# Performance work log

Hardware: AMD Instinct MI355X
Metric: run time of the kernel (lower is better)

## Reference

```python
import jax, jax.numpy as jnp
import numpy as np

B, T, C, H = 4, 2048, 1024, 16
D = C // H
SCALE = float(np.sqrt(C / H))  # quadf_scale = sqrt(D) = 8.0


def setup_inputs() -> dict:
    key = jax.random.key(0)
    k1, k2, k3 = jax.random.split(key, 3)
    x = jax.random.normal(k1, (B, T, C), dtype=jnp.float32)
    # torch Linear(C, 3C): y = x @ W.T; we store the transposed weight [C, 3C]
    W_attn = jax.random.normal(k2, (C, 3 * C), dtype=jnp.float32) * 0.02
    W_proj = jax.random.normal(k3, (C, C), dtype=jnp.float32) * 0.02
    return {"x": x, "W_attn": W_attn, "W_proj": W_proj}


def reference(x, W_attn, W_proj):
    # QKV projection
    qkv = x @ W_attn                      # [B, T, 3C]
    q, k, v = jnp.split(qkv, 3, axis=-1)  # each [B, T, C]

    def heads(t):  # [B, T, C] -> [B, H, T, D]
        return t.reshape(B, T, H, D).transpose(0, 2, 1, 3)

    q, k, v = heads(q), heads(k), heads(v)

    # scaled dot-product scores with causal mask
    scores = jnp.einsum("bhtd,bhsd->bhts", q, k) / SCALE  # [B, H, T, T]
    causal = jnp.tril(jnp.ones((T, T), dtype=bool))
    scores = jnp.where(causal, scores, -jnp.inf)
    attn = jax.nn.softmax(scores, axis=-1)
    # dropout = 0.0 (eval mode), so omitted

    y = jnp.einsum("bhts,bhsd->bhtd", attn, v)            # [B, H, T, D]
    y = y.transpose(0, 2, 1, 3).reshape(B, T, C)
    return y @ W_proj
```

## Files before the change

kernel.cpp:

```cpp
#include <hip/hip_runtime.h>
#include <hip/hip_bf16.h>

#define B_ 4
#define T_ 2048
#define C_ 1024
#define H_ 16
#define D_ 64
#define C3 3072

typedef __bf16 bf16x8 __attribute__((ext_vector_type(8)));
typedef __bf16 bf16x4 __attribute__((ext_vector_type(4)));
typedef float f32x2 __attribute__((ext_vector_type(2)));
typedef float f32x4 __attribute__((ext_vector_type(4)));
typedef float f32x16 __attribute__((ext_vector_type(16)));
typedef unsigned u32x4 __attribute__((ext_vector_type(4)));

#define SCALE_LOG2E 0.1803368801111244f

__device__ __forceinline__ void gload_lds16(const void* g, void* lds) {
  __builtin_amdgcn_global_load_lds((const __attribute__((address_space(1))) void*)g,
                                   (__attribute__((address_space(3))) void*)lds, 16, 0, 0);
}

__device__ __forceinline__ int swz128(int row, int chunk) {
  return row * 128 + ((chunk ^ (row & 7)) << 4);
}

__device__ __forceinline__ unsigned cvt_pk_bf16(float a, float b) {
  unsigned r;
  asm("v_cvt_pk_bf16_f32 %0, %1, %2" : "=v"(r) : "v"(a), "v"(b));
  return r;
}

__device__ __forceinline__ void pl32swap(unsigned& x, unsigned& y) {
  asm volatile("v_permlane32_swap_b32 %0, %1" : "+v"(x), "+v"(y));
}

__device__ __forceinline__ float fmax3(float a, float b, float c) {
  float d;
  asm("v_max3_f32 %0, %1, %2, %3" : "=v"(d) : "v"(a), "v"(b), "v"(c));
  return d;
}

__device__ __forceinline__ f32x2 pk_add(f32x2 a, f32x2 b) {
  f32x2 d;
  asm("v_pk_add_f32 %0, %1, %2" : "=v"(d) : "v"(a), "v"(b));
  return d;
}

__global__ __launch_bounds__(256) void prep_kernel(const float* __restrict__ x,
                                                   const float* __restrict__ Wa,
                                                   const float* __restrict__ Wp,
                                                   __bf16* __restrict__ xb,
                                                   __bf16* __restrict__ wat,
                                                   __bf16* __restrict__ wpt) {
  __shared__ float tile[32][33];
  int bid = blockIdx.x, tid = threadIdx.x;
  if (bid < 8192) {
    int i = bid * 256 + tid;
    float4 v = ((const float4*)x)[i];
    bf16x4 o;
    o.x = (__bf16)v.x; o.y = (__bf16)v.y; o.z = (__bf16)v.z; o.w = (__bf16)v.w;
    ((bf16x4*)xb)[i] = o;
    return;
  }
  const float* in;
  __bf16* out;
  int N, bx, by;
  if (bid < 11264) {
    int lb = bid - 8192;
    in = Wa; out = wat; N = C3;
    bx = lb % 96; by = lb / 96;
  } else {
    int lb = bid - 11264;
    in = Wp; out = wpt; N = C_;
    bx = lb & 31; by = lb >> 5;
  }
  int K = C_;
  int kb = by * 32, nb = bx * 32;
  int tx = tid & 31, ty = tid >> 5;
#pragma unroll
  for (int i = 0; i < 4; i++) {
    int r = ty + i * 8;
    tile[r][tx] = in[(size_t)(kb + r) * N + nb + tx];
  }
  __syncthreads();
#pragma unroll
  for (int i = 0; i < 4; i++) {
    int r = ty + i * 8;
    out[(size_t)(nb + r) * K + kb + tx] = (__bf16)tile[tx][r];
  }
}

template <int MODE>
__global__ __launch_bounds__(256) void gemm_bt_kernel(const __bf16* __restrict__ A,
                                                      const __bf16* __restrict__ Bt,
                                                      __bf16* __restrict__ Cb,
                                                      float* __restrict__ Cf,
                                                      __bf16* __restrict__ vT,
                                                      int M, int N, int K) {
  __shared__ __align__(16) char lds[2][32768];
  int tid = threadIdx.x, w = tid >> 6, l = tid & 63;
  int gx = gridDim.x;
  int nwg = gx * gridDim.y;
  int orig = blockIdx.y * gx + blockIdx.x;
  int cpx = nwg >> 3;
  int swz = (orig & 7) * cpx + (orig >> 3);
  int bx = swz % gx, by = swz / gx;
  int m0 = by * 128, n0 = bx * 128;
  int wr = w >> 1, wc = w & 1;
  int lr = l & 15, lhi = l >> 4;

  int srow = l >> 3;
  int cg = (l & 7) ^ (srow & 7);

  f32x4 acc[4][4];
#pragma unroll
  for (int m = 0; m < 4; m++)
#pragma unroll
    for (int n = 0; n < 4; n++) acc[m][n] = (f32x4){0.f, 0.f, 0.f, 0.f};

  auto stage = [&](int kt, int buf) {
    int k0 = kt << 6;
    char* la = &lds[buf][0];
    char* lb = &lds[buf][16384];
#pragma unroll
    for (int jj = 0; jj < 4; jj++) {
      int q = w * 4 + jj;
      int row = q * 8 + srow;
      gload_lds16(A + (size_t)(m0 + row) * K + k0 + cg * 8, la + q * 1024);
      gload_lds16(Bt + (size_t)(n0 + row) * K + k0 + cg * 8, lb + q * 1024);
    }
  };

  int nK = K >> 6;
  stage(0, 0);

  for (int kt = 0; kt < nK; kt++) {
    int buf = kt & 1;
    __syncthreads();
    if (kt + 1 < nK) stage(kt + 1, buf ^ 1);
    char* la = &lds[buf][0];
    char* lb = &lds[buf][16384];

    bf16x8 af[4][2], bfr[4][2];
#pragma unroll
    for (int m = 0; m < 4; m++) {
      int r = wr * 64 + m * 16 + lr;
#pragma unroll
      for (int kc = 0; kc < 2; kc++)
        af[m][kc] = *(const bf16x8*)(la + swz128(r, kc * 4 + lhi));
    }
#pragma unroll
    for (int n = 0; n < 4; n++) {
      int r = wc * 64 + n * 16 + lr;
#pragma unroll
      for (int kc = 0; kc < 2; kc++)
        bfr[n][kc] = *(const bf16x8*)(lb + swz128(r, kc * 4 + lhi));
    }
#pragma unroll
    for (int kc = 0; kc < 2; kc++)
#pragma unroll
      for (int m = 0; m < 4; m++)
#pragma unroll
        for (int n = 0; n < 4; n++)
          acc[m][n] =
              __builtin_amdgcn_mfma_f32_16x16x32_bf16(af[m][kc], bfr[n][kc], acc[m][n], 0, 0, 0);
  }

  if (MODE == 2 && n0 >= 2048) {
    int bb = m0 >> 11;
    int tb = (m0 & 2047) + wr * 64 + lhi * 4;
#pragma unroll
    for (int n = 0; n < 4; n++) {
      int vcol = (n0 - 2048) + wc * 64 + n * 16 + lr;
      __bf16* vp = vT + ((size_t)bb * 1024 + vcol) * T_;
#pragma unroll
      for (int m = 0; m < 4; m++) {
        bf16x4 pv;
#pragma unroll
        for (int i = 0; i < 4; i++) pv[i] = (__bf16)acc[m][n][i];
        *(bf16x4*)(vp + tb + m * 16) = pv;
      }
    }
    return;
  }

  float oscale = (MODE == 2 && n0 < 1024) ? SCALE_LOG2E : 1.0f;
#pragma unroll
  for (int m = 0; m < 4; m++)
#pragma unroll
    for (int n = 0; n < 4; n++)
#pragma unroll
      for (int i = 0; i < 4; i++) {
        int rg = m0 + wr * 64 + m * 16 + lhi * 4 + i;
        int cg2 = n0 + wc * 64 + n * 16 + lr;
        if (MODE == 1)
          Cf[(size_t)rg * N + cg2] = acc[m][n][i];
        else
          Cb[(size_t)rg * N + cg2] = (__bf16)(acc[m][n][i] * oscale);
      }
}

__global__ __launch_bounds__(256) void attn_kernel(const __bf16* __restrict__ qkv,
                                                   const __bf16* __restrict__ vT,
                                                   __bf16* __restrict__ y) {
  __shared__ __align__(16) char lds[2][16384];
  int tid = threadIdx.x, w = tid >> 6, l = tid & 63;

  int g = blockIdx.x >> 6, bh = blockIdx.x & 63;
  int q2 = g >> 2;
  int qb = (q2 & 1) ? ((q2 == 1) ? g + 4 : g - 12) : (15 - g);
  int b = bh >> 4, h = bh & 15;
  size_t base = (size_t)b * T_ * C3;
  int lq = l & 31, hi = l >> 5;
  int qrow = qb * 128 + w * 32 + lq;
  int q0w = qb * 128 + w * 32;

  int lrow = l >> 3;
  int cg = (l & 7) ^ (lrow & 7);
  const __bf16* kptr = qkv + base + (size_t)(w * 16 + lrow) * C3 + C_ + h * D_ + cg * 8;
  const __bf16* vptr = vT + ((size_t)bh * D_ + w * 16 + lrow) * T_ + cg * 8;

  bf16x8 qf[4];
  {
    const __bf16* qp = qkv + base + (size_t)qrow * C3 + h * D_;
#pragma unroll
    for (int c = 0; c < 4; c++) qf[c] = *(const bf16x8*)(qp + c * 16 + hi * 8);
  }

  f32x16 zacc;
#pragma unroll
  for (int i = 0; i < 16; i++) zacc[i] = 0.f;
  f32x16 o[2];
  o[0] = zacc; o[1] = zacc;
  float mrun = -__builtin_inff(), lrun = 0.f;

  int nt = 2 * qb + 2;

  {
    char* kb = &lds[0][0];
    char* vb = &lds[0][8192];
    gload_lds16(kptr, kb + w * 2048);
    gload_lds16(kptr + 8 * C3, kb + w * 2048 + 1024);
    gload_lds16(vptr, vb + w * 2048);
    gload_lds16(vptr + 8 * T_, vb + w * 2048 + 1024);
  }

  for (int kt = 0; kt < nt; kt++) {
    int buf = kt & 1;
    __syncthreads();
    if (kt + 1 < nt) {
      char* kb = &lds[buf ^ 1][0];
      char* vb = &lds[buf ^ 1][8192];
      const __bf16* kp = kptr + (size_t)(kt + 1) * 64 * C3;
      const __bf16* vp = vptr + (kt + 1) * 64;
      gload_lds16(kp, kb + w * 2048);
      gload_lds16(kp + 8 * C3, kb + w * 2048 + 1024);
      gload_lds16(vp, vb + w * 2048);
      gload_lds16(vp + 8 * T_, vb + w * 2048 + 1024);
    }
    if (kt * 64 > q0w + 31) continue;
    char* kb = &lds[buf][0];
    char* vb = &lds[buf][8192];

    f32x16 s[2];
    __builtin_amdgcn_s_setprio(1);
#pragma unroll
    for (int b2 = 0; b2 < 2; b2++) {
      bf16x8 kf0 = *(const bf16x8*)(kb + swz128(b2 * 32 + lq, hi));
      s[b2] = __builtin_amdgcn_mfma_f32_32x32x16_bf16(kf0, qf[0], zacc, 0, 0, 0);
#pragma unroll
      for (int c = 1; c < 4; c++) {
        bf16x8 kf = *(const bf16x8*)(kb + swz128(b2 * 32 + lq, 2 * c + hi));
        s[b2] = __builtin_amdgcn_mfma_f32_32x32x16_bf16(kf, qf[c], s[b2], 0, 0, 0);
      }
    }
    __builtin_amdgcn_s_setprio(0);

    if (kt * 64 + 63 > q0w) {
#pragma unroll
      for (int b2 = 0; b2 < 2; b2++)
#pragma unroll
        for (int r = 0; r < 16; r++) {
          int kv = kt * 64 + b2 * 32 + ((r & 3) + 8 * (r >> 2)) + 4 * hi;
          if (kv > qrow) s[b2][r] = -1e30f;
        }
    }

    {
      auto xi = [&](int i) -> float { return i < 16 ? s[0][i] : s[1][i - 16]; };
      float t10[11];
#pragma unroll
      for (int g3 = 0; g3 < 10; g3++) t10[g3] = fmax3(xi(3 * g3), xi(3 * g3 + 1), xi(3 * g3 + 2));
      t10[10] = fmaxf(xi(30), xi(31));
      float u0 = fmax3(t10[0], t10[1], t10[2]);
      float u1 = fmax3(t10[3], t10[4], t10[5]);
      float u2 = fmax3(t10[6], t10[7], t10[8]);
      float u3 = fmaxf(t10[9], t10[10]);
      float tl = fmaxf(fmax3(u0, u1, u2), u3);
      float tmax = fmaxf(tl, __shfl_xor(tl, 32));

      if (!__all(tmax - mrun <= 8.0f)) {
        float mnew = fmaxf(mrun, tmax);
        float al = __builtin_amdgcn_exp2f(mrun - mnew);
        mrun = mnew;
        lrun *= al;
#pragma unroll
        for (int d = 0; d < 2; d++)
#pragma unroll
          for (int i = 0; i < 16; i++) o[d][i] *= al;
      }
    }

#pragma unroll
    for (int b2 = 0; b2 < 2; b2++)
#pragma unroll
      for (int r = 0; r < 16; r++) s[b2][r] = __builtin_amdgcn_exp2f(s[b2][r] - mrun);

    {
      f32x2 p8[8];
#pragma unroll
      for (int g3 = 0; g3 < 8; g3++) {
        f32x2 a = {s[0][2 * g3], s[0][2 * g3 + 1]};
        f32x2 b2v = {s[1][2 * g3], s[1][2 * g3 + 1]};
        p8[g3] = pk_add(a, b2v);
      }
#pragma unroll
      for (int g3 = 0; g3 < 4; g3++) p8[g3] = pk_add(p8[g3], p8[g3 + 4]);
      p8[0] = pk_add(p8[0], p8[2]);
      p8[1] = pk_add(p8[1], p8[3]);
      p8[0] = pk_add(p8[0], p8[1]);
      float rs = p8[0][0] + p8[0][1];
      lrun += rs + __shfl_xor(rs, 32);
    }

    bf16x8 pa[4];
#pragma unroll
    for (int b2 = 0; b2 < 2; b2++) {
      unsigned wg[4][2];
#pragma unroll
      for (int gg = 0; gg < 4; gg++) {
        wg[gg][0] = cvt_pk_bf16(s[b2][4 * gg + 0], s[b2][4 * gg + 1]);
        wg[gg][1] = cvt_pk_bf16(s[b2][4 * gg + 2], s[b2][4 * gg + 3]);
      }
#pragma unroll
      for (int cp = 0; cp < 2; cp++) {
        unsigned x0 = wg[2 * cp][0], x1 = wg[2 * cp][1];
        unsigned y0 = wg[2 * cp + 1][0], y1 = wg[2 * cp + 1][1];
        pl32swap(x0, y0);
        pl32swap(x1, y1);
        union { u32x4 u; bf16x8 hh; } uu;
        uu.u = (u32x4){x0, x1, y0, y1};
        pa[b2 * 2 + cp] = uu.hh;
      }
    }

    __builtin_amdgcn_s_setprio(1);
#pragma unroll
    for (int db = 0; db < 2; db++)
#pragma unroll
      for (int c = 0; c < 4; c++) {
        bf16x8 vf = *(const bf16x8*)(vb + swz128(db * 32 + lq, 2 * c + hi));
        o[db] = __builtin_amdgcn_mfma_f32_32x32x16_bf16(vf, pa[c], o[db], 0, 0, 0);
      }
    __builtin_amdgcn_s_setprio(0);
  }

  float inv = 1.f / lrun;
  __bf16* yp = y + (size_t)(b * T_ + qrow) * C_ + h * D_;
#pragma unroll
  for (int db = 0; db < 2; db++)
#pragma unroll
    for (int rr = 0; rr < 4; rr++) {
      bf16x4 ov;
#pragma unroll
      for (int i = 0; i < 4; i++) ov[i] = (__bf16)(o[db][rr * 4 + i] * inv);
      *(bf16x4*)(yp + db * 32 + rr * 8 + hi * 4) = ov;
    }
}

extern "C" void kernel_launch(void* const* d_in, const int* in_sizes, int n_in,
                              void* d_out, int out_size, void* d_ws, size_t ws_size,
                              hipStream_t stream) {
  const float* x = (const float*)d_in[0];
  const float* Wa = (const float*)d_in[1];
  const float* Wp = (const float*)d_in[2];
  float* out = (float*)d_out;
  char* ws = (char*)d_ws;

  __bf16* xb  = (__bf16*)(ws);
  __bf16* yb  = (__bf16*)(ws);
  __bf16* wat = (__bf16*)(ws + 16777216);
  __bf16* wpt = (__bf16*)(ws + 23068672);
  __bf16* qkv = (__bf16*)(ws + 25165824);
  __bf16* vT  = (__bf16*)(ws + 75497472);

  prep_kernel<<<12288, 256, 0, stream>>>(x, Wa, Wp, xb, wat, wpt);

  gemm_bt_kernel<2><<<dim3(C3 / 128, (B_ * T_) / 128), 256, 0, stream>>>(
      xb, wat, qkv, nullptr, vT, B_ * T_, C3, C_);

  attn_kernel<<<dim3(1024), 256, 0, stream>>>(qkv, vT, yb);

  gemm_bt_kernel<1><<<dim3(C_ / 128, (B_ * T_) / 128), 256, 0, stream>>>(
      yb, wpt, nullptr, out, nullptr, B_ * T_, C_, C_);
}
```

Before: 151.7 us.

## Restructure attention into paired causal query tiles with smaller two-wave blocks

The attention kernel now uses 128-thread blocks that each process two 64-row query tiles (j and 31-j), so every block does the same amount of causal work. This replaces the 128-row tiles over four waves and the remapped block order. The double-buffered K/V prefetch is dropped: each tile is loaded into a single LDS buffer with a synchronous load, bracketed by two barriers. Blocks are also interleaved across XCDs by a bid remap. The intent is better load balance and occupancy, at the cost of exposing global load latency with no overlap and loading each K/V tile for only 64 query rows.

```diff
diff --git a/kernel.cpp b/kernel.cpp
--- a/kernel.cpp
+++ b/kernel.cpp
@@ -202,182 +202,170 @@
       }
 }
 
-__global__ __launch_bounds__(256) void attn_kernel(const __bf16* __restrict__ qkv,
+__global__ __launch_bounds__(128) void attn_kernel(const __bf16* __restrict__ qkv,
                                                    const __bf16* __restrict__ vT,
                                                    __bf16* __restrict__ y) {
-  __shared__ __align__(16) char lds[2][16384];
+  __shared__ __align__(16) char lds[16384];
   int tid = threadIdx.x, w = tid >> 6, l = tid & 63;
-
-  int g = blockIdx.x >> 6, bh = blockIdx.x & 63;
-  int q2 = g >> 2;
-  int qb = (q2 & 1) ? ((q2 == 1) ? g + 4 : g - 12) : (15 - g);
-  int b = bh >> 4, h = bh & 15;
+  int bid = blockIdx.x;
+  int lin = (bid & 7) * 128 + (bid >> 3);
+  int j = lin & 15, bh = lin >> 4, b = bh >> 4, h = bh & 15;
   size_t base = (size_t)b * T_ * C3;
   int lq = l & 31, hi = l >> 5;
-  int qrow = qb * 128 + w * 32 + lq;
-  int q0w = qb * 128 + w * 32;
 
   int lrow = l >> 3;
   int cg = (l & 7) ^ (lrow & 7);
-  const __bf16* kptr = qkv + base + (size_t)(w * 16 + lrow) * C3 + C_ + h * D_ + cg * 8;
-  const __bf16* vptr = vT + ((size_t)bh * D_ + w * 16 + lrow) * T_ + cg * 8;
-
-  bf16x8 qf[4];
-  {
-    const __bf16* qp = qkv + base + (size_t)qrow * C3 + h * D_;
-#pragma unroll
-    for (int c = 0; c < 4; c++) qf[c] = *(const bf16x8*)(qp + c * 16 + hi * 8);
-  }
+  const __bf16* kbase = qkv + base + (size_t)(w * 32 + lrow) * C3 + C_ + h * D_ + cg * 8;
+  const __bf16* vbase = vT + ((size_t)bh * D_ + w * 32 + lrow) * T_ + cg * 8;
+  char* kb = lds;
+  char* vb = lds + 8192;
 
   f32x16 zacc;
 #pragma unroll
   for (int i = 0; i < 16; i++) zacc[i] = 0.f;
-  f32x16 o[2];
-  o[0] = zacc; o[1] = zacc;
-  float mrun = -__builtin_inff(), lrun = 0.f;
-
-  int nt = 2 * qb + 2;
-
-  {
-    char* kb = &lds[0][0];
-    char* vb = &lds[0][8192];
-    gload_lds16(kptr, kb + w * 2048);
-    gload_lds16(kptr + 8 * C3, kb + w * 2048 + 1024);
-    gload_lds16(vptr, vb + w * 2048);
-    gload_lds16(vptr + 8 * T_, vb + w * 2048 + 1024);
-  }
-
-  for (int kt = 0; kt < nt; kt++) {
-    int buf = kt & 1;
-    __syncthreads();
-    if (kt + 1 < nt) {
-      char* kb = &lds[buf ^ 1][0];
-      char* vb = &lds[buf ^ 1][8192];
-      const __bf16* kp = kptr + (size_t)(kt + 1) * 64 * C3;
-      const __bf16* vp = vptr + (kt + 1) * 64;
-      gload_lds16(kp, kb + w * 2048);
-      gload_lds16(kp + 8 * C3, kb + w * 2048 + 1024);
-      gload_lds16(vp, vb + w * 2048);
-      gload_lds16(vp + 8 * T_, vb + w * 2048 + 1024);
-    }
-    if (kt * 64 > q0w + 31) continue;
-    char* kb = &lds[buf][0];
-    char* vb = &lds[buf][8192];
-
-    f32x16 s[2];
-    __builtin_amdgcn_s_setprio(1);
-#pragma unroll
-    for (int b2 = 0; b2 < 2; b2++) {
-      bf16x8 kf0 = *(const bf16x8*)(kb + swz128(b2 * 32 + lq, hi));
-      s[b2] = __builtin_amdgcn_mfma_f32_32x32x16_bf16(kf0, qf[0], zacc, 0, 0, 0);
-#pragma unroll
-      for (int c = 1; c < 4; c++) {
-        bf16x8 kf = *(const bf16x8*)(kb + swz128(b2 * 32 + lq, 2 * c + hi));
-        s[b2] = __builtin_amdgcn_mfma_f32_32x32x16_bf16(kf, qf[c], s[b2], 0, 0, 0);
-      }
-    }
-    __builtin_amdgcn_s_setprio(0);
-
-    if (kt * 64 + 63 > q0w) {
+
+#pragma unroll 1
+  for (int pi = 0; pi < 2; pi++) {
+    int p = pi ? (31 - j) : j;
+    int qrow = p * 64 + w * 32 + lq;
+
+    bf16x8 qf[4];
+    {
+      const __bf16* qp = qkv + base + (size_t)qrow * C3 + h * D_;
+#pragma unroll
+      for (int c = 0; c < 4; c++) qf[c] = *(const bf16x8*)(qp + c * 16 + hi * 8);
+    }
+
+    f32x16 o[2];
+    o[0] = zacc; o[1] = zacc;
+    float mrun = -__builtin_inff(), lrun = 0.f;
+
+#pragma unroll 1
+    for (int kt = 0; kt <= p; kt++) {
+      __syncthreads();
+#pragma unroll
+      for (int jj = 0; jj < 4; jj++) {
+        gload_lds16(kbase + (size_t)(kt * 64 + jj * 8) * C3, kb + w * 4096 + jj * 1024);
+        gload_lds16(vbase + (size_t)(jj * 8) * T_ + kt * 64, vb + w * 4096 + jj * 1024);
+      }
+      __syncthreads();
+
+      f32x16 s[2];
+      __builtin_amdgcn_s_setprio(1);
+#pragma unroll
+      for (int b2 = 0; b2 < 2; b2++) {
+        bf16x8 kf0 = *(const bf16x8*)(kb + swz128(b2 * 32 + lq, hi));
+        s[b2] = __builtin_amdgcn_mfma_f32_32x32x16_bf16(kf0, qf[0], zacc, 0, 0, 0);
+#pragma unroll
+        for (int c = 1; c < 4; c++) {
+          bf16x8 kf = *(const bf16x8*)(kb + swz128(b2 * 32 + lq, 2 * c + hi));
+          s[b2] = __builtin_amdgcn_mfma_f32_32x32x16_bf16(kf, qf[c], s[b2], 0, 0, 0);
+        }
+      }
+      __builtin_amdgcn_s_setprio(0);
+
+      if (kt == p) {
+#pragma unroll
+        for (int b2 = 0; b2 < 2; b2++)
+#pragma unroll
+          for (int r = 0; r < 16; r++) {
+            int kv = kt * 64 + b2 * 32 + ((r & 3) + 8 * (r >> 2)) + 4 * hi;
+            if (kv > qrow) s[b2][r] = -1e30f;
+          }
+      }
+
+      {
+        auto xi = [&](int i) -> float { return i < 16 ? s[0][i] : s[1][i - 16]; };
+        float t10[11];
+#pragma unroll
+        for (int g3 = 0; g3 < 10; g3++)
+          t10[g3] = fmax3(xi(3 * g3), xi(3 * g3 + 1), xi(3 * g3 + 2));
+        t10[10] = fmaxf(xi(30), xi(31));
+        float u0 = fmax3(t10[0], t10[1], t10[2]);
+        float u1 = fmax3(t10[3], t10[4], t10[5]);
+        float u2 = fmax3(t10[6], t10[7], t10[8]);
+        float u3 = fmaxf(t10[9], t10[10]);
+        float tl = fmaxf(fmax3(u0, u1, u2), u3);
+        float tmax = fmaxf(tl, __shfl_xor(tl, 32));
+
+        if (!__all(tmax - mrun <= 8.0f)) {
+          float mnew = fmaxf(mrun, tmax);
+          float al = __builtin_amdgcn_exp2f(mrun - mnew);
+          mrun = mnew;
+          lrun *= al;
+#pragma unroll
+          for (int d = 0; d < 2; d++)
+#pragma unroll
+            for (int i = 0; i < 16; i++) o[d][i] *= al;
+        }
+      }
+
 #pragma unroll
       for (int b2 = 0; b2 < 2; b2++)
 #pragma unroll
-        for (int r = 0; r < 16; r++) {
-          int kv = kt * 64 + b2 * 32 + ((r & 3) + 8 * (r >> 2)) + 4 * hi;
-          if (kv > qrow) s[b2][r] = -1e30f;
-        }
-    }
-
-    {
-      auto xi = [&](int i) -> float { return i < 16 ? s[0][i] : s[1][i - 16]; };
-      float t10[11];
-#pragma unroll
-      for (int g3 = 0; g3 < 10; g3++) t10[g3] = fmax3(xi(3 * g3), xi(3 * g3 + 1), xi(3 * g3 + 2));
-      t10[10] = fmaxf(xi(30), xi(31));
-      float u0 = fmax3(t10[0], t10[1], t10[2]);
-      float u1 = fmax3(t10[3], t10[4], t10[5]);
-      float u2 = fmax3(t10[6], t10[7], t10[8]);
-      float u3 = fmaxf(t10[9], t10[10]);
-      float tl = fmaxf(fmax3(u0, u1, u2), u3);
-      float tmax = fmaxf(tl, __shfl_xor(tl, 32));
-
-      if (!__all(tmax - mrun <= 8.0f)) {
-        float mnew = fmaxf(mrun, tmax);
-        float al = __builtin_amdgcn_exp2f(mrun - mnew);
-        mrun = mnew;
-        lrun *= al;
-#pragma unroll
-        for (int d = 0; d < 2; d++)
-#pragma unroll
-          for (int i = 0; i < 16; i++) o[d][i] *= al;
-      }
-    }
-
-#pragma unroll
-    for (int b2 = 0; b2 < 2; b2++)
-#pragma unroll
-      for (int r = 0; r < 16; r++) s[b2][r] = __builtin_amdgcn_exp2f(s[b2][r] - mrun);
-
-    {
-      f32x2 p8[8];
-#pragma unroll
-      for (int g3 = 0; g3 < 8; g3++) {
-        f32x2 a = {s[0][2 * g3], s[0][2 * g3 + 1]};
-        f32x2 b2v = {s[1][2 * g3], s[1][2 * g3 + 1]};
-        p8[g3] = pk_add(a, b2v);
-      }
-#pragma unroll
-      for (int g3 = 0; g3 < 4; g3++) p8[g3] = pk_add(p8[g3], p8[g3 + 4]);
-      p8[0] = pk_add(p8[0], p8[2]);
-      p8[1] = pk_add(p8[1], p8[3]);
-      p8[0] = pk_add(p8[0], p8[1]);
-      float rs = p8[0][0] + p8[0][1];
-      lrun += rs + __shfl_xor(rs, 32);
-    }
-
-    bf16x8 pa[4];
-#pragma unroll
-    for (int b2 = 0; b2 < 2; b2++) {
-      unsigned wg[4][2];
-#pragma unroll
-      for (int gg = 0; gg < 4; gg++) {
-        wg[gg][0] = cvt_pk_bf16(s[b2][4 * gg + 0], s[b2][4 * gg + 1]);
-        wg[gg][1] = cvt_pk_bf16(s[b2][4 * gg + 2], s[b2][4 * gg + 3]);
-      }
-#pragma unroll
-      for (int cp = 0; cp < 2; cp++) {
-        unsigned x0 = wg[2 * cp][0], x1 = wg[2 * cp][1];
-        unsigned y0 = wg[2 * cp + 1][0], y1 = wg[2 * cp + 1][1];
-        pl32swap(x0, y0);
-        pl32swap(x1, y1);
-        union { u32x4 u; bf16x8 hh; } uu;
-        uu.u = (u32x4){x0, x1, y0, y1};
-        pa[b2 * 2 + cp] = uu.hh;
-      }
-    }
-
-    __builtin_amdgcn_s_setprio(1);
+        for (int r = 0; r < 16; r++) s[b2][r] = __builtin_amdgcn_exp2f(s[b2][r] - mrun);
+
+      {
+        f32x2 p8[8];
+#pragma unroll
+        for (int g3 = 0; g3 < 8; g3++) {
+          f32x2 a = {s[0][2 * g3], s[0][2 * g3 + 1]};
+          f32x2 b2v = {s[1][2 * g3], s[1][2 * g3 + 1]};
+          p8[g3] = pk_add(a, b2v);
+        }
+#pragma unroll
+        for (int g3 = 0; g3 < 4; g3++) p8[g3] = pk_add(p8[g3], p8[g3 + 4]);
+        p8[0] = pk_add(p8[0], p8[2]);
+        p8[1] = pk_add(p8[1], p8[3]);
+        p8[0] = pk_add(p8[0], p8[1]);
+        float rs = p8[0][0] + p8[0][1];
+        lrun += rs + __shfl_xor(rs, 32);
+      }
+
+      bf16x8 pa[4];
+#pragma unroll
+      for (int b2 = 0; b2 < 2; b2++) {
+        unsigned wg[4][2];
+#pragma unroll
+        for (int gg = 0; gg < 4; gg++) {
+          wg[gg][0] = cvt_pk_bf16(s[b2][4 * gg + 0], s[b2][4 * gg + 1]);
+          wg[gg][1] = cvt_pk_bf16(s[b2][4 * gg + 2], s[b2][4 * gg + 3]);
+        }
+#pragma unroll
+        for (int cp = 0; cp < 2; cp++) {
+          unsigned x0 = wg[2 * cp][0], x1 = wg[2 * cp][1];
+          unsigned y0 = wg[2 * cp + 1][0], y1 = wg[2 * cp + 1][1];
+          pl32swap(x0, y0);
+          pl32swap(x1, y1);
+          union { u32x4 u; bf16x8 hh; } uu;
+          uu.u = (u32x4){x0, x1, y0, y1};
+          pa[b2 * 2 + cp] = uu.hh;
+        }
+      }
+
+      __builtin_amdgcn_s_setprio(1);
+#pragma unroll
+      for (int db = 0; db < 2; db++)
+#pragma unroll
+        for (int c = 0; c < 4; c++) {
+          bf16x8 vf = *(const bf16x8*)(vb + swz128(db * 32 + lq, 2 * c + hi));
+          o[db] = __builtin_amdgcn_mfma_f32_32x32x16_bf16(vf, pa[c], o[db], 0, 0, 0);
+        }
+      __builtin_amdgcn_s_setprio(0);
+    }
+
+    float inv = 1.f / lrun;
+    __bf16* yp = y + (size_t)(b * T_ + qrow) * C_ + h * D_;
 #pragma unroll
     for (int db = 0; db < 2; db++)
 #pragma unroll
-      for (int c = 0; c < 4; c++) {
-        bf16x8 vf = *(const bf16x8*)(vb + swz128(db * 32 + lq, 2 * c + hi));
-        o[db] = __builtin_amdgcn_mfma_f32_32x32x16_bf16(vf, pa[c], o[db], 0, 0, 0);
-      }
-    __builtin_amdgcn_s_setprio(0);
-  }
-
-  float inv = 1.f / lrun;
-  __bf16* yp = y + (size_t)(b * T_ + qrow) * C_ + h * D_;
-#pragma unroll
-  for (int db = 0; db < 2; db++)
-#pragma unroll
-    for (int rr = 0; rr < 4; rr++) {
-      bf16x4 ov;
-#pragma unroll
-      for (int i = 0; i < 4; i++) ov[i] = (__bf16)(o[db][rr * 4 + i] * inv);
-      *(bf16x4*)(yp + db * 32 + rr * 8 + hi * 4) = ov;
-    }
+      for (int rr = 0; rr < 4; rr++) {
+        bf16x4 ov;
+#pragma unroll
+        for (int i = 0; i < 4; i++) ov[i] = (__bf16)(o[db][rr * 4 + i] * inv);
+        *(bf16x4*)(yp + db * 32 + rr * 8 + hi * 4) = ov;
+      }
+  }
 }
 
 extern "C" void kernel_launch(void* const* d_in, const int* in_sizes, int n_in,
@@ -401,7 +389,7 @@
   gemm_bt_kernel<2><<<dim3(C3 / 128, (B_ * T_) / 128), 256, 0, stream>>>(
       xb, wat, qkv, nullptr, vT, B_ * T_, C3, C_);
 
-  attn_kernel<<<dim3(1024), 256, 0, stream>>>(qkv, vT, yb);
+  attn_kernel<<<dim3(1024), 128, 0, stream>>>(qkv, vT, yb);
 
   gemm_bt_kernel<1><<<dim3(C_ / 128, (B_ * T_) / 128), 256, 0, stream>>>(
       yb, wpt, nullptr, out, nullptr, B_ * T_, C_, C_);
```

New measurement: 164.8 us. 8.6% more time.

## Add 256x256-tile 8-wave QKV GEMM with phased async LDS pipeline

Applied to the files above, without the earlier changes.

Replaces the 128x128 QKV projection GEMM with a dedicated 512-thread kernel using 256x256 output tiles, 128KB LDS double buffering, and fine-grained per-quadrant staging with explicit vmcnt waits and setprio around MFMA blocks. Larger tiles raise arithmetic intensity and cut global/L2 traffic per FLOP, and the interleaved schedule overlaps loads with MFMA. The grid shrinks to 12x32=384 workgroups with one block per CU due to LDS use, which risks lower occupancy and tail imbalance. The output projection GEMM is simplified to fp32-only.

```diff
diff --git a/kernel.cpp b/kernel.cpp
--- a/kernel.cpp
+++ b/kernel.cpp
@@ -92,12 +92,147 @@
   }
 }
 
-template <int MODE>
+__global__ __launch_bounds__(512) void gemm_qkv256_kernel(const __bf16* __restrict__ A,
+                                                          const __bf16* __restrict__ Bt,
+                                                          __bf16* __restrict__ Cb,
+                                                          __bf16* __restrict__ vT,
+                                                          int M, int N, int K) {
+  __shared__ __align__(16) char lds[131072];
+  int tid = threadIdx.x, w = tid >> 6, l = tid & 63;
+  int wm = w >> 2, wn = w & 3;
+  int lr = l & 15, lhi = l >> 4;
+
+  int gx = gridDim.x;
+  int nwg = gx * gridDim.y;
+  int orig = blockIdx.y * gx + blockIdx.x;
+  int cpx = nwg >> 3;
+  int swz = (orig & 7) * cpx + (orig >> 3);
+  int bx = swz % gx, by = swz / gx;
+  int m0 = by * 256, n0 = bx * 256;
+
+  const __bf16* Abase = A + (size_t)m0 * K;
+  const __bf16* Bbase = Bt + (size_t)n0 * K;
+
+  f32x4 acc[8][4];
+#pragma unroll
+  for (int m = 0; m < 8; m++)
+#pragma unroll
+    for (int n = 0; n < 4; n++) acc[m][n] = (f32x4){0.f, 0.f, 0.f, 0.f};
+
+  int nKtot = K >> 6;
+  int lrow = l >> 3;
+  int cgs = (l & 7) ^ lrow;
+
+  auto stageu = [&](int u, int kt, int bufb) {
+    if (kt >= nKtot) kt = nKtot - 1;
+    int k0 = kt << 6;
+    char* dA = lds + bufb * 65536;
+    char* dB = dA + 32768;
+#pragma unroll
+    for (int jj = 0; jj < 2; jj++) {
+      int j = w * 2 + jj;
+      if (u == 0 || u == 3) {
+        int q = (u == 3);
+        int rowbase = (j >> 3) * 128 + q * 64 + (j & 7) * 8;
+        gload_lds16(Abase + (size_t)(rowbase + lrow) * K + k0 + cgs * 8, dA + rowbase * 128);
+      } else {
+        int q = (u == 2);
+        int rowbase = (j >> 2) * 64 + q * 32 + (j & 3) * 8;
+        gload_lds16(Bbase + (size_t)(rowbase + lrow) * K + k0 + cgs * 8, dB + rowbase * 128);
+      }
+    }
+  };
+
+  stageu(0, 0, 0);
+  stageu(1, 0, 0);
+  stageu(2, 0, 0);
+  stageu(3, 0, 0);
+  asm volatile("s_waitcnt vmcnt(4)" ::: "memory");
+  __builtin_amdgcn_s_barrier();
+
+  int nIter = nKtot >> 1;
+  for (int it = 0; it < nIter; it++) {
+    int tS1 = 2 * it + 1;
+    int tS2 = 2 * it + 2;
+#pragma unroll
+    for (int ph = 0; ph < 8; ph++) {
+      const int grp = ph >> 2;
+      const int sub = ph & 3;
+      const int QM = sub >> 1, QN = sub & 1;
+      if (sub == 0)      asm volatile("s_waitcnt vmcnt(4)" ::: "memory");
+      else if (sub == 1) asm volatile("s_waitcnt vmcnt(6)" ::: "memory");
+      else if (sub == 2) asm volatile("s_waitcnt vmcnt(6)" ::: "memory");
+      char* lA = lds + grp * 65536;
+      char* lB = lA + 32768;
+      bf16x8 af[4][2], bfr[2][2];
+#pragma unroll
+      for (int mf = 0; mf < 4; mf++)
+#pragma unroll
+        for (int kk = 0; kk < 2; kk++)
+          af[mf][kk] =
+              *(const bf16x8*)(lA + swz128(wm * 128 + QM * 64 + mf * 16 + lr, kk * 4 + lhi));
+#pragma unroll
+      for (int nf = 0; nf < 2; nf++)
+#pragma unroll
+        for (int kk = 0; kk < 2; kk++)
+          bfr[nf][kk] =
+              *(const bf16x8*)(lB + swz128(wn * 64 + QN * 32 + nf * 16 + lr, kk * 4 + lhi));
+      {
+        int tS = grp == 0 ? tS1 : tS2;
+        int dstb = grp == 0 ? 1 : 0;
+        if (sub == 0) { stageu(0, tS, dstb); stageu(1, tS, dstb); }
+        else if (sub == 1) stageu(2, tS, dstb);
+        else if (sub == 2) stageu(3, tS, dstb);
+      }
+      __builtin_amdgcn_s_barrier();
+      __builtin_amdgcn_s_setprio(1);
+#pragma unroll
+      for (int kk = 0; kk < 2; kk++)
+#pragma unroll
+        for (int mf = 0; mf < 4; mf++)
+#pragma unroll
+          for (int nf = 0; nf < 2; nf++)
+            acc[QM * 4 + mf][QN * 2 + nf] = __builtin_amdgcn_mfma_f32_16x16x32_bf16(
+                af[mf][kk], bfr[nf][kk], acc[QM * 4 + mf][QN * 2 + nf], 0, 0, 0);
+      __builtin_amdgcn_s_setprio(0);
+      __builtin_amdgcn_s_barrier();
+    }
+  }
+
+  if (n0 >= 2048) {
+    int bb = m0 >> 11;
+    int tb = (m0 & 2047) + wm * 128 + lhi * 4;
+#pragma unroll
+    for (int n = 0; n < 4; n++) {
+      int vcol = (n0 - 2048) + wn * 64 + n * 16 + lr;
+      __bf16* vp = vT + ((size_t)bb * 1024 + vcol) * T_;
+#pragma unroll
+      for (int m = 0; m < 8; m++) {
+        bf16x4 pv;
+#pragma unroll
+        for (int i = 0; i < 4; i++) pv[i] = (__bf16)acc[m][n][i];
+        *(bf16x4*)(vp + tb + m * 16) = pv;
+      }
+    }
+    return;
+  }
+
+  float oscale = (n0 < 1024) ? SCALE_LOG2E : 1.0f;
+#pragma unroll
+  for (int m = 0; m < 8; m++)
+#pragma unroll
+    for (int n = 0; n < 4; n++)
+#pragma unroll
+      for (int i = 0; i < 4; i++) {
+        int rg = m0 + wm * 128 + m * 16 + lhi * 4 + i;
+        int cg2 = n0 + wn * 64 + n * 16 + lr;
+        Cb[(size_t)rg * N + cg2] = (__bf16)(acc[m][n][i] * oscale);
+      }
+}
+
 __global__ __launch_bounds__(256) void gemm_bt_kernel(const __bf16* __restrict__ A,
                                                       const __bf16* __restrict__ Bt,
-                                                      __bf16* __restrict__ Cb,
                                                       float* __restrict__ Cf,
-                                                      __bf16* __restrict__ vT,
                                                       int M, int N, int K) {
   __shared__ __align__(16) char lds[2][32768];
   int tid = threadIdx.x, w = tid >> 6, l = tid & 63;
@@ -168,25 +303,6 @@
               __builtin_amdgcn_mfma_f32_16x16x32_bf16(af[m][kc], bfr[n][kc], acc[m][n], 0, 0, 0);
   }
 
-  if (MODE == 2 && n0 >= 2048) {
-    int bb = m0 >> 11;
-    int tb = (m0 & 2047) + wr * 64 + lhi * 4;
-#pragma unroll
-    for (int n = 0; n < 4; n++) {
-      int vcol = (n0 - 2048) + wc * 64 + n * 16 + lr;
-      __bf16* vp = vT + ((size_t)bb * 1024 + vcol) * T_;
-#pragma unroll
-      for (int m = 0; m < 4; m++) {
-        bf16x4 pv;
-#pragma unroll
-        for (int i = 0; i < 4; i++) pv[i] = (__bf16)acc[m][n][i];
-        *(bf16x4*)(vp + tb + m * 16) = pv;
-      }
-    }
-    return;
-  }
-
-  float oscale = (MODE == 2 && n0 < 1024) ? SCALE_LOG2E : 1.0f;
 #pragma unroll
   for (int m = 0; m < 4; m++)
 #pragma unroll
@@ -195,10 +311,7 @@
       for (int i = 0; i < 4; i++) {
         int rg = m0 + wr * 64 + m * 16 + lhi * 4 + i;
         int cg2 = n0 + wc * 64 + n * 16 + lr;
-        if (MODE == 1)
-          Cf[(size_t)rg * N + cg2] = acc[m][n][i];
-        else
-          Cb[(size_t)rg * N + cg2] = (__bf16)(acc[m][n][i] * oscale);
+        Cf[(size_t)rg * N + cg2] = acc[m][n][i];
       }
 }
 
@@ -398,11 +511,11 @@
 
   prep_kernel<<<12288, 256, 0, stream>>>(x, Wa, Wp, xb, wat, wpt);
 
-  gemm_bt_kernel<2><<<dim3(C3 / 128, (B_ * T_) / 128), 256, 0, stream>>>(
-      xb, wat, qkv, nullptr, vT, B_ * T_, C3, C_);
+  gemm_qkv256_kernel<<<dim3(C3 / 256, (B_ * T_) / 256), 512, 0, stream>>>(
+      xb, wat, qkv, vT, B_ * T_, C3, C_);
 
   attn_kernel<<<dim3(1024), 256, 0, stream>>>(qkv, vT, yb);
 
-  gemm_bt_kernel<1><<<dim3(C_ / 128, (B_ * T_) / 128), 256, 0, stream>>>(
-      yb, wpt, nullptr, out, nullptr, B_ * T_, C_, C_);
-}
+  gemm_bt_kernel<<<dim3(C_ / 128, (B_ * T_) / 128), 256, 0, stream>>>(
+      yb, wpt, out, B_ * T_, C_, C_);
+}
```

New measurement: 165.6 us. +9.2%, slower.

## Split attention into 64-row query blocks with two-wave workgroups

Applied to the files above, without the earlier changes.

Reorganizes the causal attention kernel from 1024 workgroups of 4 waves (128 query rows) to 2048 workgroups of 2 waves (64 query rows). Each wave now loads twice as much K/V per tile, and the per-wave skip of fully masked tiles is dropped because tile counts match the query block exactly. Blocks are ordered longest-first with a simpler scheduling map. The aim is finer-grained load balance and less wasted work on masked tiles, at the cost of K/V tiles being reloaded by twice as many workgroups.

```diff
diff --git a/kernel.cpp b/kernel.cpp
--- a/kernel.cpp
+++ b/kernel.cpp
@@ -202,25 +202,23 @@
       }
 }
 
-__global__ __launch_bounds__(256) void attn_kernel(const __bf16* __restrict__ qkv,
+__global__ __launch_bounds__(128) void attn_kernel(const __bf16* __restrict__ qkv,
                                                    const __bf16* __restrict__ vT,
                                                    __bf16* __restrict__ y) {
   __shared__ __align__(16) char lds[2][16384];
   int tid = threadIdx.x, w = tid >> 6, l = tid & 63;
-
-  int g = blockIdx.x >> 6, bh = blockIdx.x & 63;
-  int q2 = g >> 2;
-  int qb = (q2 & 1) ? ((q2 == 1) ? g + 4 : g - 12) : (15 - g);
+  int p = 31 - (blockIdx.x >> 6);
+  int bh = blockIdx.x & 63;
   int b = bh >> 4, h = bh & 15;
   size_t base = (size_t)b * T_ * C3;
   int lq = l & 31, hi = l >> 5;
-  int qrow = qb * 128 + w * 32 + lq;
-  int q0w = qb * 128 + w * 32;
+  int qrow = p * 64 + w * 32 + lq;
+  int q0w = p * 64 + w * 32;
 
   int lrow = l >> 3;
   int cg = (l & 7) ^ (lrow & 7);
-  const __bf16* kptr = qkv + base + (size_t)(w * 16 + lrow) * C3 + C_ + h * D_ + cg * 8;
-  const __bf16* vptr = vT + ((size_t)bh * D_ + w * 16 + lrow) * T_ + cg * 8;
+  const __bf16* kptr = qkv + base + (size_t)(w * 32 + lrow) * C3 + C_ + h * D_ + cg * 8;
+  const __bf16* vptr = vT + ((size_t)bh * D_ + w * 32 + lrow) * T_ + cg * 8;
 
   bf16x8 qf[4];
   {
@@ -236,17 +234,19 @@
   o[0] = zacc; o[1] = zacc;
   float mrun = -__builtin_inff(), lrun = 0.f;
 
-  int nt = 2 * qb + 2;
+  int nt = p + 1;
 
   {
     char* kb = &lds[0][0];
     char* vb = &lds[0][8192];
-    gload_lds16(kptr, kb + w * 2048);
-    gload_lds16(kptr + 8 * C3, kb + w * 2048 + 1024);
-    gload_lds16(vptr, vb + w * 2048);
-    gload_lds16(vptr + 8 * T_, vb + w * 2048 + 1024);
-  }
-
+#pragma unroll
+    for (int jj = 0; jj < 4; jj++) {
+      gload_lds16(kptr + (size_t)(jj * 8) * C3, kb + w * 4096 + jj * 1024);
+      gload_lds16(vptr + (size_t)(jj * 8) * T_, vb + w * 4096 + jj * 1024);
+    }
+  }
+
+#pragma unroll 1
   for (int kt = 0; kt < nt; kt++) {
     int buf = kt & 1;
     __syncthreads();
@@ -255,12 +255,12 @@
       char* vb = &lds[buf ^ 1][8192];
       const __bf16* kp = kptr + (size_t)(kt + 1) * 64 * C3;
       const __bf16* vp = vptr + (kt + 1) * 64;
-      gload_lds16(kp, kb + w * 2048);
-      gload_lds16(kp + 8 * C3, kb + w * 2048 + 1024);
-      gload_lds16(vp, vb + w * 2048);
-      gload_lds16(vp + 8 * T_, vb + w * 2048 + 1024);
-    }
-    if (kt * 64 > q0w + 31) continue;
+#pragma unroll
+      for (int jj = 0; jj < 4; jj++) {
+        gload_lds16(kp + (size_t)(jj * 8) * C3, kb + w * 4096 + jj * 1024);
+        gload_lds16(vp + (size_t)(jj * 8) * T_, vb + w * 4096 + jj * 1024);
+      }
+    }
     char* kb = &lds[buf][0];
     char* vb = &lds[buf][8192];
 
@@ -401,7 +401,7 @@
   gemm_bt_kernel<2><<<dim3(C3 / 128, (B_ * T_) / 128), 256, 0, stream>>>(
       xb, wat, qkv, nullptr, vT, B_ * T_, C3, C_);
 
-  attn_kernel<<<dim3(1024), 256, 0, stream>>>(qkv, vT, yb);
+  attn_kernel<<<dim3(2048), 128, 0, stream>>>(qkv, vT, yb);
 
   gemm_bt_kernel<1><<<dim3(C_ / 128, (B_ * T_) / 128), 256, 0, stream>>>(
       yb, wpt, nullptr, out, nullptr, B_ * T_, C_, C_);
```

Measured after the change: 161.7 us. 6.6% more time.
